# Performance work log

Hardware: AMD Instinct MI355X
Metric: run time of the kernel (lower is better)

Reference implementation:

```python
import jax, jax.numpy as jnp
import numpy as np

MAX_DIST = 5
D_PE = 16
NUM_ENTITIES = 50000
NUM_EDGES = 800000
NUM_ANCHOR_TRIPLES = 32
MAX_SOURCES = 2 * NUM_ANCHOR_TRIPLES  # upper bound on unique anchor entities


def setup_inputs() -> dict:
    key = jax.random.key(0)
    k1, k2, k3, k4 = jax.random.split(key, 4)
    h_ids = jax.random.randint(k1, (NUM_EDGES,), 0, NUM_ENTITIES)
    t_ids = jax.random.randint(k2, (NUM_EDGES,), 0, NUM_ENTITIES)
    anchor_triple_indices = jax.random.randint(k3, (NUM_ANCHOR_TRIPLES,), 0, NUM_EDGES)
    dist_embed = jax.random.normal(k4, (MAX_DIST + 1, D_PE), dtype=jnp.float32)
    return {
        "h_ids": h_ids,
        "t_ids": t_ids,
        "anchor_triple_indices": anchor_triple_indices,
        "num_entities": NUM_ENTITIES,
        "dist_embed": dist_embed,
    }


def _bfs_mean_counts(h_ids, t_ids, anchor_triple_indices, num_entities):
    """Returns [num_entities, MAX_DIST+1] mean one-hot distance counts over anchors."""
    # unique anchor entities, padded with -1 to a static size (torch.unique equivalent)
    anchor_ents = jnp.concatenate([h_ids[anchor_triple_indices], t_ids[anchor_triple_indices]])
    sources = jnp.unique(anchor_ents, size=MAX_SOURCES, fill_value=-1)  # [K], sorted
    valid = sources >= 0                                                # [K]
    src = jnp.where(valid, sources, 0)
    K = src.shape[0]
    col = jnp.arange(K)

    # symmetric adjacency as edge list (duplicates are harmless: only >0 is tested)
    edge_src = jnp.concatenate([h_ids, t_ids])  # [2E]
    edge_dst = jnp.concatenate([t_ids, h_ids])  # [2E]

    frontier = jnp.zeros((num_entities, K), jnp.float32).at[src, col].set(1.0)
    visited = jnp.zeros((num_entities, K), bool).at[src, col].set(True)
    dist = jnp.full((num_entities, K), MAX_DIST, jnp.int32).at[src, col].set(0)

    for depth in range(1, MAX_DIST + 1):  # fixed small hop count
        # sparse adj @ frontier == scatter-add of gathered frontier rows
        new_frontier = jax.ops.segment_sum(frontier[edge_src], edge_dst, num_segments=num_entities)
        newly = (new_frontier > 0) & ~visited
        dist = jnp.where(newly, depth, dist)
        visited = visited | newly
        frontier = newly.astype(jnp.float32)

    # masked mean over valid anchor sources, expressed as distance-count histogram
    w = valid.astype(jnp.float32)
    n_valid = jnp.maximum(w.sum(), 1.0)
    onehot = jax.nn.one_hot(dist, MAX_DIST + 1, dtype=jnp.float32)  # [N, K, D+1]
    counts = jnp.einsum('nkd,k->nd', onehot, w) / n_valid           # [N, D+1]
    return counts


def reference(h_ids, t_ids, anchor_triple_indices, num_entities, dist_embed):
    counts = _bfs_mean_counts(h_ids, t_ids, anchor_triple_indices, num_entities)
    # mean over sources of embed(dist) == counts @ embedding table
    return counts @ dist_embed  # [num_entities, d_pe]
```

## Files before the change

kernel.cpp:

```cpp
#include <hip/hip_runtime.h>
#include <hip/hip_bf16.h>

typedef unsigned long long u64;
typedef unsigned int u32;
typedef unsigned short u16;

#define MAXD 5
#define BSH  6
#define BN   64
#define NW   512
#define NTH  256
#define CAPG 2816
#define HEMPTY 0xFFFFFFFFu


__global__ __launch_bounds__(NTH) void chunk_sort(
    const int* __restrict__ h, const int* __restrict__ t, int E, int CE, int CAPC,
    int NB, u32* __restrict__ recs, u16* __restrict__ segtab,
    const int* __restrict__ anchor, int A,
    u64* __restrict__ NFg, u32* __restrict__ srcPack, int* __restrict__ nvalid) {
    extern __shared__ u64 dyn[];
    u64* edl   = dyn;
    u32* buf   = (u32*)(edl + CE);
    u32* offs  = buf + CAPC;
    u32* cur   = offs + NB;
    u32* hsKey = cur + NB;
    u32* hsBit = hsKey + 128;
    u32* waveSum = hsBit + 128;
    int tid = threadIdx.x, c = blockIdx.x;
    int lane = tid & 63, w = tid >> 6;
    int lo = c * CE, hi = min(E, lo + CE);
    int ne = hi - lo;
    int nrec = 2 * ne;

    for (int i = tid; i < ne; i += NTH)
        edl[i] = ((u64)(u32)h[lo + i] << 32) | (u32)t[lo + i];
    for (int i = tid; i < NB; i += NTH) cur[i] = 0u;
    if (tid < 128) hsKey[tid] = HEMPTY;
    __syncthreads();

    if (tid < 64) {
        int K = 2 * A;
        int a_ = (tid < K) ? anchor[(tid < A) ? tid : (tid - A)] : 0;
        int my = (tid < K) ? ((tid < A) ? h[a_] : t[a_]) : -1;
        bool uniq = (tid < K);
        for (int j = 0; j < 64; ++j) {
            int o = __shfl(my, j, 64);
            if (j < tid && o == my) uniq = false;
        }
        u64 mask = __ballot(uniq);
        if (c == 0 && tid == 0) *nvalid = (int)__popcll(mask);
        if (uniq) {
            u32 slot = ((u32)my * 2654435761u) >> 25;
            while (atomicCAS(&hsKey[slot], HEMPTY, (u32)my) != HEMPTY)
                slot = (slot + 1) & 127u;
            hsBit[slot] = (u32)tid;
        }
        if (c == 0)
            srcPack[tid] = uniq ? (((u32)my << BSH) | (u32)tid) : HEMPTY;
    }

    for (int i = tid; i < ne; i += NTH) {
        u64 e = edl[i];
        u32 uu = (u32)(e >> 32), vv = (u32)e;
        atomicAdd(&cur[vv >> BSH], 1u);
        atomicAdd(&cur[uu >> BSH], 1u);
    }
    __syncthreads();

    {
        u32 i0 = (u32)tid * 4;
        u32 aa[4];
#pragma unroll
        for (int k = 0; k < 4; ++k) {
            u32 i = i0 + k;
            aa[k] = (i < (u32)NB) ? cur[i] : 0u;
        }
        u32 sum = aa[0] + aa[1] + aa[2] + aa[3];
        u32 p = sum;
#pragma unroll
        for (int d = 1; d < 64; d <<= 1) {
            u32 x = (u32)__shfl_up((int)p, d, 64);
            if (lane >= d) p += x;
        }
        u32 excl = p - sum;
        if (lane == 63) waveSum[w] = p;
        __syncthreads();
        u32 woff = 0;
        for (int k = 0; k < w; ++k) woff += waveSum[k];
        u32 o0 = woff + excl;
        u32 o1 = o0 + aa[0], o2 = o1 + aa[1], o3 = o2 + aa[2];
        u32 oo[4] = {o0, o1, o2, o3};
#pragma unroll
        for (int k = 0; k < 4; ++k) {
            u32 i = i0 + k;
            if (i < (u32)NB) {
                offs[i] = oo[k];
                segtab[c * (NB + 1) + i] = (u16)oo[k];
                cur[i] = 0u;
            }
        }
        if (tid == 0) segtab[c * (NB + 1) + NB] = (u16)nrec;
    }
    __syncthreads();

    auto srcMask = [&](u32 src) -> u64 {
        u32 slot = (src * 2654435761u) >> 25;
        while (true) {
            u32 k = hsKey[slot];
            if (k == src) return 1ull << hsBit[slot];
            if (k == HEMPTY) return 0ull;
            slot = (slot + 1) & 127u;
        }
    };

    for (int i = tid; i < ne; i += NTH) {
        u64 e = edl[i];
        u32 uu = (u32)(e >> 32), vv = (u32)e;
        u32 b1 = vv >> BSH;
        buf[offs[b1] + atomicAdd(&cur[b1], 1u)] = (uu << BSH) | (vv & (BN - 1));
        u32 b2 = uu >> BSH;
        buf[offs[b2] + atomicAdd(&cur[b2], 1u)] = (vv << BSH) | (uu & (BN - 1));
        if (uu != vv) {
            u64 m1 = srcMask(uu);
            if (m1) atomicOr(&NFg[vv], m1);
            u64 m2 = srcMask(vv);
            if (m2) atomicOr(&NFg[uu], m2);
        }
    }
    __syncthreads();
    for (int i = tid; i < nrec; i += NTH) recs[c * CAPC + i] = buf[i];
}

__global__ __launch_bounds__(NTH) void level12_merge(
    const u32* __restrict__ recs, const u16* __restrict__ segtab, int CAPC, int NB,
    const u32* __restrict__ srcPack, const u64* __restrict__ NFg,
    u64* __restrict__ F2, u64* __restrict__ V, u64* __restrict__ CNT,
    u32* __restrict__ recs2, u32* __restrict__ bucketCnt, int N) {
    __shared__ u32 s0a[NW];
    __shared__ u32 loff[NW + 1];
    __shared__ u32 waveSum[4];
    __shared__ u32 buf[CAPG];
    __shared__ u64 NF[BN];
    __shared__ u32 srcL[64];
    int b = blockIdx.x, tid = threadIdx.x;
    int lane = tid & 63, w = tid >> 6;
    if (tid < BN) NF[tid] = 0ull;
    if (tid < 64) srcL[tid] = srcPack[tid];

    u32 c0 = 2 * tid, c1 = 2 * tid + 1;
    u32 a0 = segtab[c0 * (NB + 1) + b], e0 = segtab[c0 * (NB + 1) + b + 1];
    u32 a1 = segtab[c1 * (NB + 1) + b], e1 = segtab[c1 * (NB + 1) + b + 1];
    s0a[c0] = a0;
    s0a[c1] = a1;
    u32 l0 = e0 - a0, l1 = e1 - a1;
    u32 sum = l0 + l1;
    u32 p = sum;
#pragma unroll
    for (int d = 1; d < 64; d <<= 1) {
        u32 x = (u32)__shfl_up((int)p, d, 64);
        if (lane >= d) p += x;
    }
    u32 excl = p - sum;
    if (lane == 63) waveSum[w] = p;
    __syncthreads();
    u32 woff = 0;
    for (int k = 0; k < w; ++k) woff += waveSum[k];
    u32 base = woff + excl;
    loff[c0] = base;
    loff[c1] = base + l0;
    if (tid == NTH - 1) loff[NW] = base + l0 + l1;
    __syncthreads();

    u32 T = min(loff[NW], (u32)CAPG);

    u32 per = (T + NTH - 1) / NTH;
    u32 j0 = min((u32)tid * per, T), j1 = min(j0 + per, T);
    if (j0 < j1) {
        int c = 0;
#pragma unroll
        for (int step = 256; step >= 1; step >>= 1)
            if (c + step <= NW - 1 && loff[c + step] <= j0) c += step;
        for (u32 j = j0; j < j1; ++j) {
            while (loff[c + 1] <= j) ++c;
            buf[j] = recs[(u32)c * CAPC + s0a[c] + (j - loff[c])];
        }
    }
    __syncthreads();

    u32 o0 = (u32)b * CAPG;
    u32 r = tid;
    for (; r + 3u * NTH < T; r += 4u * NTH) {
        u32 r0 = buf[r],           r1 = buf[r + NTH];
        u32 r2 = buf[r + 2 * NTH], r3 = buf[r + 3 * NTH];
        recs2[o0 + r] = r0;
        recs2[o0 + r + NTH] = r1;
        recs2[o0 + r + 2 * NTH] = r2;
        recs2[o0 + r + 3 * NTH] = r3;
        u64 f0 = NFg[r0 >> BSH], f1 = NFg[r1 >> BSH];
        u64 f2 = NFg[r2 >> BSH], f3 = NFg[r3 >> BSH];
        if (f0) atomicOr(&NF[r0 & (BN - 1)], f0);
        if (f1) atomicOr(&NF[r1 & (BN - 1)], f1);
        if (f2) atomicOr(&NF[r2 & (BN - 1)], f2);
        if (f3) atomicOr(&NF[r3 & (BN - 1)], f3);
    }
    for (; r < T; r += NTH) {
        u32 r0 = buf[r];
        recs2[o0 + r] = r0;
        u64 f0 = NFg[r0 >> BSH];
        if (f0) atomicOr(&NF[r0 & (BN - 1)], f0);
    }
    __syncthreads();
    if (tid == 0) bucketCnt[b] = T;
    if (tid < BN) {
        int n = b * BN + tid;
        if (n < N) {
            u64 srcbit = 0ull;
            for (int k = 0; k < 64; ++k) {
                u32 pk = srcL[k];
                if (pk != HEMPTY && (int)(pk >> BSH) == n)
                    srcbit |= 1ull << (pk & (BN - 1));
            }
            u64 nf1 = NFg[n];
            u64 v1 = srcbit | nf1;
            u64 newly2 = NF[tid] & ~v1;
            V[n] = v1 | newly2;
            F2[n] = newly2;
            CNT[n] = (srcbit ? 1ull : 0ull)
                   | ((u64)__popcll(nf1) << 8)
                   | ((u64)__popcll(newly2) << 16);
        }
    }
}

__global__ __launch_bounds__(NTH) void level3(
    const u32* __restrict__ recs2, const u32* __restrict__ bucketCnt,
    const u64* __restrict__ Fin, u64* __restrict__ Fout,
    u64* __restrict__ V, u64* __restrict__ CNT, int N) {
    __shared__ u64 NF[BN];
    int b = blockIdx.x, tid = threadIdx.x;
    u32 o0 = (u32)b * CAPG;
    u32 cnt = bucketCnt[b];
    if (tid < BN) NF[tid] = 0ull;
    __syncthreads();
    u32 r = tid;
    for (; r + 3u * NTH < cnt; r += 4u * NTH) {
        u32 c0 = recs2[o0 + r],           c1 = recs2[o0 + r + NTH];
        u32 c2 = recs2[o0 + r + 2 * NTH], c3 = recs2[o0 + r + 3 * NTH];
        u64 f0 = Fin[c0 >> BSH], f1 = Fin[c1 >> BSH];
        u64 f2 = Fin[c2 >> BSH], f3 = Fin[c3 >> BSH];
        if (f0) atomicOr(&NF[c0 & (BN - 1)], f0);
        if (f1) atomicOr(&NF[c1 & (BN - 1)], f1);
        if (f2) atomicOr(&NF[c2 & (BN - 1)], f2);
        if (f3) atomicOr(&NF[c3 & (BN - 1)], f3);
    }
    for (; r < cnt; r += NTH) {
        u32 c0 = recs2[o0 + r];
        u64 f0 = Fin[c0 >> BSH];
        if (f0) atomicOr(&NF[c0 & (BN - 1)], f0);
    }
    __syncthreads();
    if (tid < BN) {
        int n = b * BN + tid;
        if (n < N) {
            u64 vis = V[n];
            u64 newly = NF[tid] & ~vis;
            Fout[n] = newly;
            if (newly) {
                V[n] = vis | newly;
                CNT[n] += (u64)__popcll(newly) << 24;
            }
        }
    }
}

__global__ __launch_bounds__(NTH) void level4_fin(
    const u32* __restrict__ recs2, const u32* __restrict__ bucketCnt,
    const u64* __restrict__ Fin, const u64* __restrict__ V,
    const u64* __restrict__ CNT, const int* __restrict__ nvalid,
    const float* __restrict__ embed, float* __restrict__ out, int N) {
    __shared__ u64 NF[BN];
    int b = blockIdx.x, tid = threadIdx.x;
    u32 o0 = (u32)b * CAPG;
    u32 cnt = bucketCnt[b];
    if (tid < BN) NF[tid] = 0ull;
    __syncthreads();
    u32 r = tid;
    for (; r + 3u * NTH < cnt; r += 4u * NTH) {
        u32 c0 = recs2[o0 + r],           c1 = recs2[o0 + r + NTH];
        u32 c2 = recs2[o0 + r + 2 * NTH], c3 = recs2[o0 + r + 3 * NTH];
        u64 f0 = Fin[c0 >> BSH], f1 = Fin[c1 >> BSH];
        u64 f2 = Fin[c2 >> BSH], f3 = Fin[c3 >> BSH];
        if (f0) atomicOr(&NF[c0 & (BN - 1)], f0);
        if (f1) atomicOr(&NF[c1 & (BN - 1)], f1);
        if (f2) atomicOr(&NF[c2 & (BN - 1)], f2);
        if (f3) atomicOr(&NF[c3 & (BN - 1)], f3);
    }
    for (; r < cnt; r += NTH) {
        u32 c0 = recs2[o0 + r];
        u64 f0 = Fin[c0 >> BSH];
        if (f0) atomicOr(&NF[c0 & (BN - 1)], f0);
    }
    __syncthreads();
    int nl = tid >> 2, q = tid & 3;
    int n = b * BN + nl;
    if (n >= N) return;
    u64 vis = V[n];
    int c4 = __popcll(NF[nl] & ~vis);
    u64 c = CNT[n];
    int nv = *nvalid;
    float inv = 1.0f / (float)(nv > 0 ? nv : 1);
    float cd[MAXD + 1];
    int total = c4;
#pragma unroll
    for (int d = 0; d < 4; ++d) {
        int x = (int)((c >> (8 * d)) & 0xffull);
        total += x;
        cd[d] = (float)x;
    }
    cd[4] = (float)c4;
    cd[5] = (float)(nv - total);

    const float4* e4 = (const float4*)embed;
    float4 acc = {0.f, 0.f, 0.f, 0.f};
#pragma unroll
    for (int d = 0; d <= MAXD; ++d) {
        float4 e = e4[d * 4 + q];
        acc.x += cd[d] * e.x; acc.y += cd[d] * e.y;
        acc.z += cd[d] * e.z; acc.w += cd[d] * e.w;
    }
    acc.x *= inv; acc.y *= inv; acc.z *= inv; acc.w *= inv;
    ((float4*)(out + (size_t)n * 16))[q] = acc;
}

extern "C" void kernel_launch(void* const* d_in, const int* in_sizes, int n_in,
                              void* d_out, int out_size, void* d_ws, size_t ws_size,
                              hipStream_t stream) {
    const int*   h      = (const int*)d_in[0];
    const int*   t      = (const int*)d_in[1];
    const int*   anchor = (const int*)d_in[2];
    const float* embed  = (const float*)d_in[4];
    float*       out    = (float*)d_out;

    int E = in_sizes[0];
    int A = in_sizes[2];
    int D = in_sizes[4] / (MAXD + 1);
    int N = out_size / D;
    int NB = (N + BN - 1) >> BSH;
    int CE = (E + NW - 1) / NW;
    int CAPC = 2 * CE;
    (void)D;

    u64* NFg = (u64*)d_ws;
    u64* V   = NFg + N;
    u64* CNT = V + N;
    u64* F2  = CNT + N;
    u64* F3  = F2 + N;
    u32* srcPack   = (u32*)(F3 + N);
    int* nvalid    = (int*)(srcPack + 64);
    u32* bucketCnt = (u32*)(nvalid + 1);
    u32* recs      = bucketCnt + NB;
    u16* segtab    = (u16*)(recs + (size_t)NW * CAPC);
    u32* recs2     = (u32*)(segtab + (size_t)NW * (NB + 1));

    hipMemsetAsync(NFg, 0, (size_t)N * 8, stream);

    size_t shmem = (size_t)CE * 8
                 + (size_t)(CAPC + NB + NB + 128 + 128 + 4) * sizeof(u32);
    chunk_sort<<<NW, NTH, shmem, stream>>>(h, t, E, CE, CAPC, NB, recs, segtab,
                                           anchor, A, NFg, srcPack, nvalid);

    level12_merge<<<NB, NTH, 0, stream>>>(recs, segtab, CAPC, NB, srcPack, NFg,
                                          F2, V, CNT, recs2, bucketCnt, N);
    level3<<<NB, NTH, 0, stream>>>(recs2, bucketCnt, F2, F3, V, CNT, N);
    level4_fin<<<NB, NTH, 0, stream>>>(recs2, bucketCnt, F3, V, CNT,
                                       nvalid, embed, out, N);
}
```

Measured before the change: 138.0 us.

## Double chunk count and drop shared-memory edge staging in chunk sort

Raises the number of edge chunks from 512 to 1024, so chunk_sort launches more, smaller blocks and the merge kernel gathers from four chunks per thread instead of two. The shared-memory copy of each chunk's edges is removed, and h/t are read from global memory twice instead, which cuts dynamic LDS use and allows more blocks per CU. In exchange the merge does a deeper binary search, reads more segment-table entries per bucket, and chunk_sort issues repeated global loads.

```diff
diff --git a/kernel.cpp b/kernel.cpp
--- a/kernel.cpp
+++ b/kernel.cpp
@@ -8,7 +8,7 @@
 #define MAXD 5
 #define BSH  6
 #define BN   64
-#define NW   512
+#define NW   1024
 #define NTH  256
 #define CAPG 2816
 #define HEMPTY 0xFFFFFFFFu
@@ -19,9 +19,8 @@
     int NB, u32* __restrict__ recs, u16* __restrict__ segtab,
     const int* __restrict__ anchor, int A,
     u64* __restrict__ NFg, u32* __restrict__ srcPack, int* __restrict__ nvalid) {
-    extern __shared__ u64 dyn[];
-    u64* edl   = dyn;
-    u32* buf   = (u32*)(edl + CE);
+    extern __shared__ u32 sh[];
+    u32* buf   = sh;
     u32* offs  = buf + CAPC;
     u32* cur   = offs + NB;
     u32* hsKey = cur + NB;
@@ -33,8 +32,6 @@
     int ne = hi - lo;
     int nrec = 2 * ne;
 
-    for (int i = tid; i < ne; i += NTH)
-        edl[i] = ((u64)(u32)h[lo + i] << 32) | (u32)t[lo + i];
     for (int i = tid; i < NB; i += NTH) cur[i] = 0u;
     if (tid < 128) hsKey[tid] = HEMPTY;
     __syncthreads();
@@ -61,8 +58,7 @@
     }
 
     for (int i = tid; i < ne; i += NTH) {
-        u64 e = edl[i];
-        u32 uu = (u32)(e >> 32), vv = (u32)e;
+        u32 uu = (u32)h[lo + i], vv = (u32)t[lo + i];
         atomicAdd(&cur[vv >> BSH], 1u);
         atomicAdd(&cur[uu >> BSH], 1u);
     }
@@ -89,8 +85,8 @@
         u32 woff = 0;
         for (int k = 0; k < w; ++k) woff += waveSum[k];
         u32 o0 = woff + excl;
-        u32 o1 = o0 + aa[0], o2 = o1 + aa[1], o3 = o2 + aa[2];
-        u32 oo[4] = {o0, o1, o2, o3};
+        u32 oo[4] = {o0, o0 + aa[0], o0 + aa[0] + aa[1],
+                     o0 + aa[0] + aa[1] + aa[2]};
 #pragma unroll
         for (int k = 0; k < 4; ++k) {
             u32 i = i0 + k;
@@ -115,8 +111,7 @@
     };
 
     for (int i = tid; i < ne; i += NTH) {
-        u64 e = edl[i];
-        u32 uu = (u32)(e >> 32), vv = (u32)e;
+        u32 uu = (u32)h[lo + i], vv = (u32)t[lo + i];
         u32 b1 = vv >> BSH;
         buf[offs[b1] + atomicAdd(&cur[b1], 1u)] = (uu << BSH) | (vv & (BN - 1));
         u32 b2 = uu >> BSH;
@@ -137,7 +132,7 @@
     const u32* __restrict__ srcPack, const u64* __restrict__ NFg,
     u64* __restrict__ F2, u64* __restrict__ V, u64* __restrict__ CNT,
     u32* __restrict__ recs2, u32* __restrict__ bucketCnt, int N) {
-    __shared__ u32 s0a[NW];
+    __shared__ u16 s0a[NW];
     __shared__ u32 loff[NW + 1];
     __shared__ u32 waveSum[4];
     __shared__ u32 buf[CAPG];
@@ -148,13 +143,18 @@
     if (tid < BN) NF[tid] = 0ull;
     if (tid < 64) srcL[tid] = srcPack[tid];
 
-    u32 c0 = 2 * tid, c1 = 2 * tid + 1;
-    u32 a0 = segtab[c0 * (NB + 1) + b], e0 = segtab[c0 * (NB + 1) + b + 1];
-    u32 a1 = segtab[c1 * (NB + 1) + b], e1 = segtab[c1 * (NB + 1) + b + 1];
-    s0a[c0] = a0;
-    s0a[c1] = a1;
-    u32 l0 = e0 - a0, l1 = e1 - a1;
-    u32 sum = l0 + l1;
+    u32 c0 = (u32)tid * 4;
+    u32 aa[4], ll[4];
+#pragma unroll
+    for (int k = 0; k < 4; ++k) {
+        u32 c = c0 + k;
+        u32 a = segtab[c * (NB + 1) + b];
+        u32 e = segtab[c * (NB + 1) + b + 1];
+        s0a[c] = (u16)a;
+        aa[k] = a;
+        ll[k] = e - a;
+    }
+    u32 sum = ll[0] + ll[1] + ll[2] + ll[3];
     u32 p = sum;
 #pragma unroll
     for (int d = 1; d < 64; d <<= 1) {
@@ -167,9 +167,12 @@
     u32 woff = 0;
     for (int k = 0; k < w; ++k) woff += waveSum[k];
     u32 base = woff + excl;
-    loff[c0] = base;
-    loff[c1] = base + l0;
-    if (tid == NTH - 1) loff[NW] = base + l0 + l1;
+    loff[c0]     = base;
+    loff[c0 + 1] = base + ll[0];
+    loff[c0 + 2] = base + ll[0] + ll[1];
+    loff[c0 + 3] = base + ll[0] + ll[1] + ll[2];
+    if (tid == NTH - 1) loff[NW] = base + sum;
+    (void)aa;
     __syncthreads();
 
     u32 T = min(loff[NW], (u32)CAPG);
@@ -179,11 +182,11 @@
     if (j0 < j1) {
         int c = 0;
 #pragma unroll
-        for (int step = 256; step >= 1; step >>= 1)
+        for (int step = 512; step >= 1; step >>= 1)
             if (c + step <= NW - 1 && loff[c + step] <= j0) c += step;
         for (u32 j = j0; j < j1; ++j) {
             while (loff[c + 1] <= j) ++c;
-            buf[j] = recs[(u32)c * CAPC + s0a[c] + (j - loff[c])];
+            buf[j] = recs[(u32)c * CAPC + (u32)s0a[c] + (j - loff[c])];
         }
     }
     __syncthreads();
@@ -365,8 +368,7 @@
 
     hipMemsetAsync(NFg, 0, (size_t)N * 8, stream);
 
-    size_t shmem = (size_t)CE * 8
-                 + (size_t)(CAPC + NB + NB + 128 + 128 + 4) * sizeof(u32);
+    size_t shmem = (size_t)(CAPC + 2 * NB + 260) * sizeof(u32);
     chunk_sort<<<NW, NTH, shmem, stream>>>(h, t, E, CE, CAPC, NB, recs, segtab,
                                            anchor, A, NFg, srcPack, nvalid);
 
```

Result: faster. 135.0 us (-2.1%).
